# Kernel optimization log

Hardware: AMD Instinct MI355X
Metric: run time of the kernel (lower is better)

Reference implementation:

```python
import jax, jax.numpy as jnp
import numpy as np

SIM_THRESHOLD = 0.7
EPS = 1e-8  # matches torch F.cosine_similarity eps

Q, M, D, C = 4096, 65536, 384, 128


def setup_inputs() -> dict:
    key = jax.random.key(0)
    k1, k2, k3 = jax.random.split(key, 3)
    query_embeddings = jax.random.normal(k1, (Q, D), dtype=jnp.float32)
    memory_embeddings = jax.random.normal(k2, (M, D), dtype=jnp.float32)
    # per-example one-hot-ish label vectors [M, C]
    memory_labels = jax.random.uniform(k3, (M, C), dtype=jnp.float32)
    return {
        "query_embeddings": query_embeddings,
        "memory_embeddings": memory_embeddings,
        "memory_labels": memory_labels,
    }


def _l2_normalize(x):
    n = jnp.sqrt(jnp.sum(x * x, axis=-1, keepdims=True))
    return x / jnp.maximum(n, EPS)


def reference(query_embeddings, memory_embeddings, memory_labels):
    # cosine similarity matrix [Q, M] via normalized GEMM
    qn = _l2_normalize(query_embeddings)          # [Q, D]
    mn = _l2_normalize(memory_embeddings)         # [M, D]
    sims = jnp.einsum("qd,md->qm", qn, mn)        # [Q, M]
    max_sim = jnp.max(sims, axis=1)               # [Q]
    max_idx = jnp.argmax(sims, axis=1)            # [Q]
    picked = memory_labels[max_idx]               # [Q, C] gather
    C_ = memory_labels.shape[1]
    uniform = jnp.full((1, C_), 1.0 / C_, dtype=picked.dtype)
    predictions = jnp.where((max_sim > SIM_THRESHOLD)[:, None], picked, uniform)
    return predictions
```

## Files before the change

kernel.cpp:

```cpp
#include <hip/hip_runtime.h>
#include <math.h>

#define QN 4096
#define MN 65536
#define DN 384
#define CN 128
#define NCHUNK 64
#define MROWS_PER_CHUNK (MN / NCHUNK)
#define MT_PER (MROWS_PER_CHUNK / 64)
#define FRAG_B 2048
#define GSTRIDE (3 * FRAG_B)
#define TSTRIDE (4 * GSTRIDE)

typedef __attribute__((ext_vector_type(8))) int i32x8;
typedef __attribute__((ext_vector_type(4))) int i32x4;
typedef __attribute__((ext_vector_type(4))) float f32x4;

__device__ __forceinline__ void async16(const void* g, void* l) {
  __builtin_amdgcn_global_load_lds(
      (const __attribute__((address_space(1))) unsigned int*)g,
      (__attribute__((address_space(3))) unsigned int*)l, 16, 0, 0);
}

__global__ __launch_bounds__(256) void nrm_kernel(const float* __restrict__ qe,
                                                  const float* __restrict__ me,
                                                  unsigned char* __restrict__ yq,
                                                  unsigned char* __restrict__ ym) {
  const int row = blockIdx.x * 4 + (threadIdx.x >> 6);
  const int lane = threadIdx.x & 63;
  const float* xr = (row < QN) ? qe + (size_t)row * DN
                               : me + (size_t)(row - QN) * DN;
  float2 v[3];
  float ss = 0.f;
#pragma unroll
  for (int i = 0; i < 3; ++i) {
    v[i] = *(const float2*)&xr[lane * 2 + i * 128];
    ss += v[i].x * v[i].x + v[i].y * v[i].y;
  }
#pragma unroll
  for (int m = 1; m < 64; m <<= 1) ss += __shfl_xor(ss, m);
  const float scale = 1.0f / fmaxf(sqrtf(ss), 1e-8f);
  if (row < QN) {
    unsigned short* yw = (unsigned short*)(yq + (size_t)row * DN);
#pragma unroll
    for (int i = 0; i < 3; ++i) {
      const int p = __builtin_amdgcn_cvt_pk_fp8_f32(v[i].x * scale,
                                                    v[i].y * scale, 0, false);
      yw[lane + i * 64] = (unsigned short)(p & 0xffff);
    }
  } else {
    const int mr = row - QN;
    const int g = mr >> 4, r15 = mr & 15;
    const int fl = ((lane >> 4) << 4) + r15;
    unsigned short* yw = (unsigned short*)ym;
#pragma unroll
    for (int i = 0; i < 3; ++i) {
      const int p = __builtin_amdgcn_cvt_pk_fp8_f32(v[i].x * scale,
                                                    v[i].y * scale, 0, false);
      yw[((size_t)(g * 3 + i) * 64 + fl) * 16 + (lane & 15)] =
          (unsigned short)(p & 0xffff);
    }
  }
}

__global__ __launch_bounds__(256, 2) void gemm_max_kernel(
    const unsigned char* __restrict__ qn8, const unsigned char* __restrict__ mn8,
    float* __restrict__ pmax) {
  __shared__ unsigned char As[128 * DN];
  __shared__ float smax[2][128];

  const int tid = threadIdx.x;
  const int wave = tid >> 6, lane = tid & 63;
  const int wr = wave >> 1, wc = wave & 1;
  const int quad = lane >> 4, l16 = lane & 15;
  const int r7 = l16 & 7;

  const int bid = blockIdx.y * gridDim.x + blockIdx.x;
  const int xcd = bid & 7;
  const int j = bid >> 3;
  const int ychunk = (xcd << 3) | (j >> 5);
  const int qrow0 = (j & 31) * 128;
  const int mchunk0 = ychunk * MROWS_PER_CHUNK;

  float rmax[16];
#pragma unroll
  for (int i = 0; i < 16; ++i) rmax[i] = -3.0e38f;

  {
    const unsigned char* abase = qn8 + (size_t)qrow0 * DN;
#pragma unroll
    for (int i = 0; i < 12; ++i) {
      const int ci = i * 256 + tid;
      const int row = ci / 24;
      const int jj = ci - row * 24;
      const int gj = (jj & 24) | ((jj ^ row) & 7);
      async16(abase + row * DN + gj * 16, &As[(i * 256 + wave * 64) * 16]);
    }
  }
  __syncthreads();
  i32x8 afr[3][4];
#pragma unroll
  for (int kc = 0; kc < 3; ++kc)
#pragma unroll
    for (int rt = 0; rt < 4; ++rt) {
      const unsigned char* p = &As[(wr * 64 + rt * 16 + l16) * DN];
      i32x4 lo = *(const i32x4*)&p[(kc * 8 + ((quad * 2 + 0) ^ r7)) * 16];
      i32x4 hi = *(const i32x4*)&p[(kc * 8 + ((quad * 2 + 1) ^ r7)) * 16];
      afr[kc][rt][0] = lo[0]; afr[kc][rt][1] = lo[1];
      afr[kc][rt][2] = lo[2]; afr[kc][rt][3] = lo[3];
      afr[kc][rt][4] = hi[0]; afr[kc][rt][5] = hi[1];
      afr[kc][rt][6] = hi[2]; afr[kc][rt][7] = hi[3];
    }

  const int g0 = (mchunk0 >> 4) + wc * 2;
  const unsigned char* bp0 = mn8 + ((size_t)g0 * 3 * 64 + lane) * 32;
  const unsigned char* bp1 = bp0 + GSTRIDE;

#pragma unroll 1
  for (int mt = 0; mt < MT_PER; ++mt) {
    i32x8 bfr[3][2];
#pragma unroll
    for (int kc = 0; kc < 3; ++kc) {
      bfr[kc][0] = *(const i32x8*)(bp0 + kc * FRAG_B);
      bfr[kc][1] = *(const i32x8*)(bp1 + kc * FRAG_B);
    }

    f32x4 acc[4][2];
#pragma unroll
    for (int rt = 0; rt < 4; ++rt)
#pragma unroll
      for (int ct = 0; ct < 2; ++ct) acc[rt][ct] = (f32x4){0.f, 0.f, 0.f, 0.f};

    __builtin_amdgcn_s_setprio(1);
#pragma unroll
    for (int kc = 0; kc < 3; ++kc)
#pragma unroll
      for (int rt = 0; rt < 4; ++rt)
#pragma unroll
        for (int ct = 0; ct < 2; ++ct)
          acc[rt][ct] = __builtin_amdgcn_mfma_scale_f32_16x16x128_f8f6f4(
              afr[kc][rt], bfr[kc][ct], acc[rt][ct], 0, 0,
              0, 0x7f7f7f7f, 0, 0x7f7f7f7f);
    __builtin_amdgcn_s_setprio(0);

#pragma unroll
    for (int rt = 0; rt < 4; ++rt)
#pragma unroll
      for (int r = 0; r < 4; ++r) {
        const float v = fmaxf(acc[rt][0][r], acc[rt][1][r]);
        rmax[rt * 4 + r] = fmaxf(rmax[rt * 4 + r], v);
      }

    bp0 += TSTRIDE;
    bp1 += TSTRIDE;
  }

#pragma unroll
  for (int i = 0; i < 16; ++i) {
    float v = rmax[i];
    v = fmaxf(v, __shfl_xor(v, 1));
    v = fmaxf(v, __shfl_xor(v, 2));
    v = fmaxf(v, __shfl_xor(v, 4));
    v = fmaxf(v, __shfl_xor(v, 8));
    rmax[i] = v;
  }
  if (l16 == 0) {
#pragma unroll
    for (int rt = 0; rt < 4; ++rt)
#pragma unroll
      for (int r = 0; r < 4; ++r)
        smax[wc][wr * 64 + rt * 16 + quad * 4 + r] = rmax[rt * 4 + r];
  }
  __syncthreads();
  if (tid < 128) {
    const float v = fmaxf(smax[0][tid], smax[1][tid]);
    pmax[(size_t)(qrow0 + tid) * NCHUNK + ychunk] = v;
  }
}

__global__ __launch_bounds__(256) void decide_kernel(
    const float* __restrict__ pmax, const float* __restrict__ qe,
    const float* __restrict__ me, const float* __restrict__ labels,
    float* __restrict__ out) {
  const int q = blockIdx.x;
  const int t = threadIdx.x;
  __shared__ float smx;
  if (t < 64) {
    float v = pmax[(size_t)q * NCHUNK + t];
#pragma unroll
    for (int m = 1; m < 64; m <<= 1) v = fmaxf(v, __shfl_xor(v, m));
    if (t == 0) smx = v;
  }
  __syncthreads();
  if (smx <= 0.5f) {
    if (t < CN) out[(size_t)q * CN + t] = 1.0f / 128.0f;
    return;
  }
  __shared__ float sred[256];
  __shared__ int sidx[256];
  __shared__ float wsum[4];
  const float* qr = qe + (size_t)q * DN;
  float ss = 0.f;
  for (int i = t; i < DN; i += 256) ss += qr[i] * qr[i];
#pragma unroll
  for (int m = 1; m < 64; m <<= 1) ss += __shfl_xor(ss, m);
  if ((t & 63) == 0) wsum[t >> 6] = ss;
  __syncthreads();
  const float qnorm = fmaxf(sqrtf(wsum[0] + wsum[1] + wsum[2] + wsum[3]), 1e-8f);

  float best = -3.0e38f;
  int bidx = 0x7fffffff;
  for (int j = t; j < MN; j += 256) {
    const float* mr = me + (size_t)j * DN;
    float dot = 0.f, ms = 0.f;
    for (int k = 0; k < DN; ++k) {
      float a = qr[k], b = mr[k];
      dot += a * b;
      ms += b * b;
    }
    const float sim = dot / (qnorm * fmaxf(sqrtf(ms), 1e-8f));
    if (sim > best) { best = sim; bidx = j; }
  }
  sred[t] = best;
  sidx[t] = bidx;
  __syncthreads();
  for (int s = 128; s > 0; s >>= 1) {
    if (t < s) {
      const float ov = sred[t + s];
      const int oi = sidx[t + s];
      if (ov > sred[t] || (ov == sred[t] && oi < sidx[t])) {
        sred[t] = ov;
        sidx[t] = oi;
      }
    }
    __syncthreads();
  }
  const float mx = sred[0];
  const int mi = sidx[0];
  if (t < CN)
    out[(size_t)q * CN + t] =
        (mx > 0.7f) ? labels[(size_t)mi * CN + t] : (1.0f / 128.0f);
}

extern "C" void kernel_launch(void* const* d_in, const int* in_sizes, int n_in,
                              void* d_out, int out_size, void* d_ws,
                              size_t ws_size, hipStream_t stream) {
  const float* qe = (const float*)d_in[0];
  const float* me = (const float*)d_in[1];
  const float* lb = (const float*)d_in[2];
  float* out = (float*)d_out;

  char* ws = (char*)d_ws;
  const size_t OFF_QN = 0;
  const size_t OFF_MN = OFF_QN + (size_t)QN * DN;
  const size_t OFF_PMAX = OFF_MN + (size_t)MN * DN;
  unsigned char* qn8 = (unsigned char*)(ws + OFF_QN);
  unsigned char* mn8 = (unsigned char*)(ws + OFF_MN);
  float* pmax = (float*)(ws + OFF_PMAX);

  nrm_kernel<<<(QN + MN) / 4, 256, 0, stream>>>(qe, me, qn8, mn8);
  gemm_max_kernel<<<dim3(QN / 128, NCHUNK), 256, 0, stream>>>(qn8, mn8, pmax);
  decide_kernel<<<QN, 256, 0, stream>>>(pmax, qe, me, lb, out);
}
```

Measured before the change: 252.1 us.

## Double-buffer B fragment loads in GEMM-max loop with explicit vmcnt waits

Replaces the per-iteration load-then-compute of memory-embedding fragments with a two-stage register double buffer (bfrA/bfrB), issuing the next tile's global loads before computing the current one. Explicit s_waitcnt vmcnt and sched_barrier calls pin the ordering so the loads overlap the MFMA work. The MFMA loop is also reordered per column tile, so only four accumulators are live at once instead of eight. The goal is to hide global load latency in the hot loop, at the cost of more live registers for the second B buffer and hand-tuned wait counts that must match the number of outstanding loads.

```diff
diff --git a/kernel.cpp b/kernel.cpp
--- a/kernel.cpp
+++ b/kernel.cpp
@@ -113,47 +113,67 @@
     }
 
   const int g0 = (mchunk0 >> 4) + wc * 2;
-  const unsigned char* bp0 = mn8 + ((size_t)g0 * 3 * 64 + lane) * 32;
-  const unsigned char* bp1 = bp0 + GSTRIDE;
+  const unsigned char* bpA0 = mn8 + ((size_t)g0 * 3 * 64 + lane) * 32;
+  const unsigned char* bpA1 = bpA0 + GSTRIDE;
+  const unsigned char* bpB0 = bpA0 + TSTRIDE;
+  const unsigned char* bpB1 = bpA1 + TSTRIDE;
+
+#define LOADB(BFR, P0, P1)                                  \
+  do {                                                      \
+    _Pragma("unroll") for (int kc = 0; kc < 3; ++kc) {      \
+      BFR[kc][0] = *(const i32x8*)((P0) + kc * FRAG_B);     \
+      BFR[kc][1] = *(const i32x8*)((P1) + kc * FRAG_B);     \
+    }                                                       \
+  } while (0)
+
+#define COMPUTE_TILE(BFR)                                                     \
+  do {                                                                        \
+    _Pragma("unroll") for (int ct = 0; ct < 2; ++ct) {                        \
+      f32x4 acc[4];                                                           \
+      _Pragma("unroll") for (int rt = 0; rt < 4; ++rt)                        \
+          acc[rt] = (f32x4){0.f, 0.f, 0.f, 0.f};                              \
+      __builtin_amdgcn_s_setprio(1);                                          \
+      _Pragma("unroll") for (int kc = 0; kc < 3; ++kc)                        \
+          _Pragma("unroll") for (int rt = 0; rt < 4; ++rt)                    \
+              acc[rt] = __builtin_amdgcn_mfma_scale_f32_16x16x128_f8f6f4(     \
+                  afr[kc][rt], BFR[kc][ct], acc[rt], 0, 0, 0, 0x7f7f7f7f, 0,  \
+                  0x7f7f7f7f);                                                \
+      __builtin_amdgcn_s_setprio(0);                                          \
+      _Pragma("unroll") for (int rt = 0; rt < 4; ++rt)                        \
+          _Pragma("unroll") for (int r = 0; r < 4; ++r)                       \
+              rmax[rt * 4 + r] = fmaxf(rmax[rt * 4 + r], acc[rt][r]);         \
+    }                                                                         \
+  } while (0)
+
+  i32x8 bfrA[3][2], bfrB[3][2];
+  LOADB(bfrA, bpA0, bpA1);
+  bpA0 += 2 * TSTRIDE; bpA1 += 2 * TSTRIDE;
+  LOADB(bfrB, bpB0, bpB1);
+  bpB0 += 2 * TSTRIDE; bpB1 += 2 * TSTRIDE;
+  asm volatile("s_waitcnt vmcnt(12)" ::: "memory");
+  __builtin_amdgcn_sched_barrier(0);
 
 #pragma unroll 1
-  for (int mt = 0; mt < MT_PER; ++mt) {
-    i32x8 bfr[3][2];
-#pragma unroll
-    for (int kc = 0; kc < 3; ++kc) {
-      bfr[kc][0] = *(const i32x8*)(bp0 + kc * FRAG_B);
-      bfr[kc][1] = *(const i32x8*)(bp1 + kc * FRAG_B);
-    }
-
-    f32x4 acc[4][2];
-#pragma unroll
-    for (int rt = 0; rt < 4; ++rt)
-#pragma unroll
-      for (int ct = 0; ct < 2; ++ct) acc[rt][ct] = (f32x4){0.f, 0.f, 0.f, 0.f};
-
-    __builtin_amdgcn_s_setprio(1);
-#pragma unroll
-    for (int kc = 0; kc < 3; ++kc)
-#pragma unroll
-      for (int rt = 0; rt < 4; ++rt)
-#pragma unroll
-        for (int ct = 0; ct < 2; ++ct)
-          acc[rt][ct] = __builtin_amdgcn_mfma_scale_f32_16x16x128_f8f6f4(
-              afr[kc][rt], bfr[kc][ct], acc[rt][ct], 0, 0,
-              0, 0x7f7f7f7f, 0, 0x7f7f7f7f);
-    __builtin_amdgcn_s_setprio(0);
-
-#pragma unroll
-    for (int rt = 0; rt < 4; ++rt)
-#pragma unroll
-      for (int r = 0; r < 4; ++r) {
-        const float v = fmaxf(acc[rt][0][r], acc[rt][1][r]);
-        rmax[rt * 4 + r] = fmaxf(rmax[rt * 4 + r], v);
-      }
-
-    bp0 += TSTRIDE;
-    bp1 += TSTRIDE;
-  }
+  for (int mt = 0; mt < MT_PER; mt += 2) {
+    COMPUTE_TILE(bfrA);
+    if (mt + 2 < MT_PER) {
+      LOADB(bfrA, bpA0, bpA1);
+      bpA0 += 2 * TSTRIDE; bpA1 += 2 * TSTRIDE;
+      asm volatile("s_waitcnt vmcnt(12)" ::: "memory");
+    } else {
+      asm volatile("s_waitcnt vmcnt(0)" ::: "memory");
+    }
+    __builtin_amdgcn_sched_barrier(0);
+    COMPUTE_TILE(bfrB);
+    if (mt + 3 < MT_PER) {
+      LOADB(bfrB, bpB0, bpB1);
+      bpB0 += 2 * TSTRIDE; bpB1 += 2 * TSTRIDE;
+      asm volatile("s_waitcnt vmcnt(12)" ::: "memory");
+      __builtin_amdgcn_sched_barrier(0);
+    }
+  }
+#undef LOADB
+#undef COMPUTE_TILE
 
 #pragma unroll
   for (int i = 0; i < 16; ++i) {
```

New measurement: 595.5 us. 2.36x slower.
